# Kernel optimization log

Hardware: AMD Instinct MI355X
Metric: run time of the kernel (lower is better)

The kernel has to match this reference:

```python
import jax, jax.numpy as jnp
import numpy as np

B, T, D = 2, 2048, 1024
N, H = 16, 64  # num_heads, head_dim
LOG2E = 1.442695041
NEG_INF = -1.0e9


def setup_inputs() -> dict:
    key = jax.random.key(0)
    ks = jax.random.split(key, 6)
    return {
        "input_tensor": jax.random.normal(ks[0], (B, T, D), dtype=jnp.float32),
        "attention_mask": jax.random.randint(ks[1], (B, 1, T, T), 0, 2, dtype=jnp.int32),
        "wq": jax.random.normal(ks[2], (D, N, H), dtype=jnp.float32),
        "bq": jnp.zeros((N, H), dtype=jnp.float32),
        "wk": jax.random.normal(ks[3], (D, N, H), dtype=jnp.float32),
        "bk": jnp.zeros((N, H), dtype=jnp.float32),
        "wv": jax.random.normal(ks[4], (D, N, H), dtype=jnp.float32),
        "bv": jnp.zeros((N, H), dtype=jnp.float32),
        "wo": jax.random.normal(ks[5], (D, N, H), dtype=jnp.float32),
        "bo": jnp.zeros((D,), dtype=jnp.float32),
        "per_dim_scale": jnp.zeros((H,), dtype=jnp.float32),
    }


def reference(input_tensor, attention_mask, wq, bq, wk, bk, wv, bv, wo, bo, per_dim_scale):
    # QKV projections: [B,T,D] x [D,N,H] -> [B,T,N,H]
    q = jnp.einsum('btd,dnh->btnh', input_tensor, wq) + bq
    k = jnp.einsum('btd,dnh->btnh', input_tensor, wk) + bk
    v = jnp.einsum('btd,dnh->btnh', input_tensor, wv) + bv
    # per-dim query scaling: (log2(e)/sqrt(H)) * softplus(per_dim_scale)
    scale = (LOG2E / jnp.sqrt(jnp.asarray(H, q.dtype))) * jax.nn.softplus(per_dim_scale)
    q = q * scale
    # scores: [B,N,T,S]
    scores = jnp.einsum('btnh,bsnh->bnts', q, k)
    scores = jnp.where(attention_mask == 0, jnp.asarray(NEG_INF, scores.dtype), scores)
    weights = jax.nn.softmax(scores, axis=-1)
    # AV: [B,N,T,S] x [B,S,N,H] -> [B,T,N,H]
    attn_out = jnp.einsum('bnts,bsnh->btnh', weights, v)
    # output projection: [B,T,N,H] x [D,N,H] -> [B,T,D]
    return jnp.einsum('btnh,dnh->btd', attn_out, wo) + bo
```

## Files before the change

### kernel.cpp

```cpp
#include <hip/hip_runtime.h>
#include <math.h>

typedef __bf16 bf16;
typedef __attribute__((ext_vector_type(8))) __bf16 bf16x8;
typedef __attribute__((ext_vector_type(4))) __bf16 bf16x4;
typedef __attribute__((ext_vector_type(4))) float f32x4;

#define BB 2
#define TT 2048
#define DD 1024
#define NHD 16
#define HD 64
#define MM (BB*TT)
#define LOG2E_F 1.442695041f
#define NEGINF_F (-1.0e9f)

__device__ __forceinline__ void gld16(const bf16* g, bf16* l)
{
    __builtin_amdgcn_global_load_lds(
        (const __attribute__((address_space(1))) unsigned int*)g,
        (__attribute__((address_space(3))) unsigned int*)l, 16, 0, 0);
}

__global__ __launch_bounds__(256)
void prep_all(const float* __restrict__ X, const int* __restrict__ m,
              const float* __restrict__ wq, const float* __restrict__ wk,
              const float* __restrict__ wv, const float* __restrict__ wo,
              bf16* __restrict__ Xh, bf16* __restrict__ Xl,
              bf16* __restrict__ qkh, bf16* __restrict__ qkl,
              bf16* __restrict__ vh, bf16* __restrict__ ob,
              unsigned char* __restrict__ bits)
{
    __shared__ float tile[32][33];
    const int bid = blockIdx.x;
    const int t   = threadIdx.x;

    if (bid < 4096) {
        int i = bid * 256 + t;
        float4 v = ((const float4*)X)[i];
        float f[4] = {v.x, v.y, v.z, v.w};
        bf16x4 h, l;
        #pragma unroll
        for (int j = 0; j < 4; ++j) {
            bf16 hh = (bf16)f[j];
            h[j] = hh;
            l[j] = (bf16)(f[j] - (float)hh);
        }
        *(bf16x4*)(Xh + (size_t)i * 4) = h;
        *(bf16x4*)(Xl + (size_t)i * 4) = l;
        return;
    }
    if (bid < 8192) {
        const int idx = bid - 4096;
        const int z   = idx >> 10;
        const int bx  = (idx & 31) << 5;
        const int by  = ((idx >> 5) & 31) << 5;
        const int r   = t >> 3;
        const int c4  = (t & 7) << 2;
        if (z == 3) {
            float4 v = *(const float4*)(wo + (size_t)(by + r) * 1024 + bx + c4);
            bf16x4 o = { (bf16)v.x, (bf16)v.y, (bf16)v.z, (bf16)v.w };
            *(bf16x4*)(ob + (size_t)(by + r) * 1024 + bx + c4) = o;
            return;
        }
        const float* src = (z == 0) ? wq : ((z == 1) ? wk : wv);
        bf16* oh = (z == 0) ? qkh : ((z == 1) ? qkh + 1048576 : vh);
        bf16* ol = (z == 0) ? qkl : ((z == 1) ? qkl + 1048576 : nullptr);
        float4 v = *(const float4*)(src + (size_t)(by + r) * 1024 + bx + c4);
        tile[r][c4+0] = v.x; tile[r][c4+1] = v.y;
        tile[r][c4+2] = v.z; tile[r][c4+3] = v.w;
        __syncthreads();
        bf16x4 hv, lv;
        #pragma unroll
        for (int j = 0; j < 4; ++j) {
            float f = tile[c4 + j][r];
            bf16 h = (bf16)f;
            hv[j] = h;
            lv[j] = (bf16)(f - (float)h);
        }
        *(bf16x4*)(oh + (size_t)(bx + r) * 1024 + by + c4) = hv;
        if (ol)
            *(bf16x4*)(ol + (size_t)(bx + r) * 1024 + by + c4) = lv;
        return;
    }
    {
        int i = (bid - 8192) * 256 + t;
        const int4* mp = (const int4*)m + (size_t)i * 2;
        int4 a  = mp[0];
        int4 b4 = mp[1];
        unsigned v = (a.x  != 0)       | ((a.y  != 0) << 1)
                   | ((a.z  != 0) << 2) | ((a.w  != 0) << 3)
                   | ((b4.x != 0) << 4) | ((b4.y != 0) << 5)
                   | ((b4.z != 0) << 6) | ((b4.w != 0) << 7);
        bits[i] = (unsigned char)v;
    }
}

__global__ __launch_bounds__(256)
void gemm_proj(const bf16* __restrict__ Xh, const bf16* __restrict__ Xl,
               const bf16* __restrict__ Wh, const bf16* __restrict__ Wl,
               const bf16* __restrict__ Wvh,
               const float* __restrict__ bq, const float* __restrict__ bk,
               const float* __restrict__ bv, const float* __restrict__ pds,
               bf16* __restrict__ oQh, bf16* __restrict__ oQl,
               bf16* __restrict__ oKh, bf16* __restrict__ oKl,
               bf16* __restrict__ oVt)
{
    __shared__ bf16 S[4][128 * 32];

    const int bid  = blockIdx.x;
    const int t    = threadIdx.x;
    const int lane = t & 63;
    const int w    = t >> 6;
    const int quad = lane >> 4, l15 = lane & 15;
    const int wm   = (w >> 1) << 6;
    const int wn   = (w & 1)  << 6;

    const int jr0 = ((w * 2 + 0) << 4) + (lane >> 2);
    const int jr1 = ((w * 2 + 1) << 4) + (lane >> 2);
    const int kch = (lane & 3) << 3;
    const int off0 = (w * 2 + 0) * 512;
    const int off1 = (w * 2 + 1) * 512;

    if (bid < 512) {
        const int m0 = (bid >> 4) << 7;
        const int n0 = (bid & 15) << 7;
        bf16* Ah = S[0]; bf16* Al = S[1]; bf16* Bh = S[2]; bf16* Bl = S[3];

        const bf16* pAh0 = Xh + (size_t)(m0 + jr0) * DD + kch;
        const bf16* pAh1 = Xh + (size_t)(m0 + jr1) * DD + kch;
        const bf16* pAl0 = Xl + (size_t)(m0 + jr0) * DD + kch;
        const bf16* pAl1 = Xl + (size_t)(m0 + jr1) * DD + kch;
        const bf16* pBh0 = Wh + (size_t)(n0 + jr0) * DD + kch;
        const bf16* pBh1 = Wh + (size_t)(n0 + jr1) * DD + kch;
        const bf16* pBl0 = Wl + (size_t)(n0 + jr0) * DD + kch;
        const bf16* pBl1 = Wl + (size_t)(n0 + jr1) * DD + kch;

        f32x4 acc[4][4] = {};

        for (int k0 = 0; k0 < DD; k0 += 32) {
            __syncthreads();
            gld16(pAh0 + k0, Ah + off0);  gld16(pAh1 + k0, Ah + off1);
            gld16(pAl0 + k0, Al + off0);  gld16(pAl1 + k0, Al + off1);
            gld16(pBh0 + k0, Bh + off0);  gld16(pBh1 + k0, Bh + off1);
            gld16(pBl0 + k0, Bl + off0);  gld16(pBl1 + k0, Bl + off1);
            __syncthreads();

            bf16x8 ah[4], bh[4];
            #pragma unroll
            for (int mt = 0; mt < 4; ++mt)
                ah[mt] = *(const bf16x8*)(Ah + (wm + (mt << 4) + l15) * 32 + (quad << 3));
            #pragma unroll
            for (int nt = 0; nt < 4; ++nt)
                bh[nt] = *(const bf16x8*)(Bh + (wn + (nt << 4) + l15) * 32 + (quad << 3));
            #pragma unroll
            for (int mt = 0; mt < 4; ++mt)
                #pragma unroll
                for (int nt = 0; nt < 4; ++nt)
                    acc[mt][nt] = __builtin_amdgcn_mfma_f32_16x16x32_bf16(
                        ah[mt], bh[nt], acc[mt][nt], 0, 0, 0);

            bf16x8 bl[4];
            #pragma unroll
            for (int nt = 0; nt < 4; ++nt)
                bl[nt] = *(const bf16x8*)(Bl + (wn + (nt << 4) + l15) * 32 + (quad << 3));
            #pragma unroll
            for (int mt = 0; mt < 4; ++mt)
                #pragma unroll
                for (int nt = 0; nt < 4; ++nt)
                    acc[mt][nt] = __builtin_amdgcn_mfma_f32_16x16x32_bf16(
                        ah[mt], bl[nt], acc[mt][nt], 0, 0, 0);

            bf16x8 al[4];
            #pragma unroll
            for (int mt = 0; mt < 4; ++mt)
                al[mt] = *(const bf16x8*)(Al + (wm + (mt << 4) + l15) * 32 + (quad << 3));
            #pragma unroll
            for (int mt = 0; mt < 4; ++mt)
                #pragma unroll
                for (int nt = 0; nt < 4; ++nt)
                    acc[mt][nt] = __builtin_amdgcn_mfma_f32_16x16x32_bf16(
                        al[mt], bh[nt], acc[mt][nt], 0, 0, 0);
        }

        #pragma unroll
        for (int nt = 0; nt < 4; ++nt) {
            const int col = n0 + wn + (nt << 4) + l15;
            const int isQ = (col < 1024);
            const int nh  = col & 1023;
            const int n   = nh >> 6, h = nh & 63;
            const float bcol = isQ ? bq[nh] : bk[nh];
            float s = 1.f;
            if (isQ) {
                float x  = pds[h];
                float sp = fmaxf(x, 0.f) + log1pf(expf(-fabsf(x)));
                s = (LOG2E_F * LOG2E_F / 8.0f) * sp;
            }
            bf16* dH = isQ ? oQh : oKh;
            bf16* dL = isQ ? oQl : oKl;
            #pragma unroll
            for (int mt = 0; mt < 4; ++mt) {
                #pragma unroll
                for (int reg = 0; reg < 4; ++reg) {
                    const int row = m0 + wm + (mt << 4) + (quad << 2) + reg;
                    const int bi  = row >> 11;
                    const int tt  = row & (TT - 1);
                    float val = (acc[mt][nt][reg] + bcol) * s;
                    const size_t idx = (((size_t)bi * NHD + n) * TT + tt) * HD + h;
                    bf16 hi = (bf16)val;
                    dH[idx] = hi;
                    dL[idx] = (bf16)(val - (float)hi);
                }
            }
        }
    } else {
        const int idx = bid - 512;
        const int m0  = (idx >> 5) << 7;
        const int n0  = (idx & 31) << 7;
        bf16* As = S[0]; bf16* Bs = S[2];

        const bf16* Ap0 = Wvh + (size_t)(m0 + jr0) * DD + kch;
        const bf16* Ap1 = Wvh + (size_t)(m0 + jr1) * DD + kch;
        const bf16* Bp0 = Xh  + (size_t)(n0 + jr0) * DD + kch;
        const bf16* Bp1 = Xh  + (size_t)(n0 + jr1) * DD + kch;

        f32x4 acc[4][4] = {};

        for (int k0 = 0; k0 < DD; k0 += 32) {
            __syncthreads();
            gld16(Ap0 + k0, As + off0);
            gld16(Ap1 + k0, As + off1);
            gld16(Bp0 + k0, Bs + off0);
            gld16(Bp1 + k0, Bs + off1);
            __syncthreads();
            bf16x8 af[4], bfm[4];
            #pragma unroll
            for (int mt = 0; mt < 4; ++mt)
                af[mt] = *(const bf16x8*)(As + (wm + (mt << 4) + l15) * 32 + (quad << 3));
            #pragma unroll
            for (int nt = 0; nt < 4; ++nt)
                bfm[nt] = *(const bf16x8*)(Bs + (wn + (nt << 4) + l15) * 32 + (quad << 3));
            #pragma unroll
            for (int mt = 0; mt < 4; ++mt)
                #pragma unroll
                for (int nt = 0; nt < 4; ++nt)
                    acc[mt][nt] = __builtin_amdgcn_mfma_f32_16x16x32_bf16(
                        af[mt], bfm[nt], acc[mt][nt], 0, 0, 0);
        }

        #pragma unroll
        for (int nt = 0; nt < 4; ++nt) {
            const int col = n0 + wn + (nt << 4) + l15;
            const int bi  = col >> 11;
            const int tt  = col & (TT - 1);
            #pragma unroll
            for (int mt = 0; mt < 4; ++mt) {
                #pragma unroll
                for (int reg = 0; reg < 4; ++reg) {
                    const int row = m0 + wm + (mt << 4) + (quad << 2) + reg;
                    float val = acc[mt][nt][reg] + bv[row];
                    oVt[((size_t)bi * 1024 + row) * TT + tt] = (bf16)val;
                }
            }
        }
    }
}

__global__ __launch_bounds__(256)
void gemm_out(const bf16* __restrict__ A, const bf16* __restrict__ Bt,
              const float* __restrict__ bias, float* __restrict__ oF)
{
    __shared__ bf16 As[128 * 32];
    __shared__ bf16 Bs[64 * 32];

    const int t    = threadIdx.x;
    const int lane = t & 63;
    const int w    = t >> 6;
    const int quad = lane >> 4, l15 = lane & 15;
    const int m0   = blockIdx.y << 7;
    const int n0   = blockIdx.x << 6;
    const int wm   = (w >> 1) << 6;
    const int wn   = (w & 1)  << 5;

    const int jr0 = ((w * 2 + 0) << 4) + (lane >> 2);
    const int jr1 = ((w * 2 + 1) << 4) + (lane >> 2);
    const int jrB = (w << 4) + (lane >> 2);
    const int kch = (lane & 3) << 3;

    bf16* lA0 = As + (w * 2 + 0) * 512;
    bf16* lA1 = As + (w * 2 + 1) * 512;
    bf16* lB  = Bs + w * 512;

    const bf16* Ap0 = A  + (size_t)(m0 + jr0) * DD + kch;
    const bf16* Ap1 = A  + (size_t)(m0 + jr1) * DD + kch;
    const bf16* Bp  = Bt + (size_t)(n0 + jrB) * DD + kch;

    f32x4 acc[4][2] = {};

    for (int k0 = 0; k0 < DD; k0 += 32) {
        __syncthreads();
        gld16(Ap0 + k0, lA0);
        gld16(Ap1 + k0, lA1);
        gld16(Bp + k0, lB);
        __syncthreads();
        bf16x8 af[4], bfm[2];
        #pragma unroll
        for (int mt = 0; mt < 4; ++mt)
            af[mt] = *(const bf16x8*)(As + (wm + (mt << 4) + l15) * 32 + (quad << 3));
        #pragma unroll
        for (int nt = 0; nt < 2; ++nt)
            bfm[nt] = *(const bf16x8*)(Bs + (wn + (nt << 4) + l15) * 32 + (quad << 3));
        #pragma unroll
        for (int mt = 0; mt < 4; ++mt)
            #pragma unroll
            for (int nt = 0; nt < 2; ++nt)
                acc[mt][nt] = __builtin_amdgcn_mfma_f32_16x16x32_bf16(
                    af[mt], bfm[nt], acc[mt][nt], 0, 0, 0);
    }

    #pragma unroll
    for (int nt = 0; nt < 2; ++nt) {
        const int col = n0 + wn + (nt << 4) + l15;
        const float bcol = bias[col];
        #pragma unroll
        for (int mt = 0; mt < 4; ++mt) {
            #pragma unroll
            for (int reg = 0; reg < 4; ++reg) {
                const int row = m0 + wm + (mt << 4) + (quad << 2) + reg;
                oF[(size_t)row * DD + col] = acc[mt][nt][reg] + bcol;
            }
        }
    }
}

__global__ __launch_bounds__(512)
void attn_mfma(const bf16* __restrict__ Qh, const bf16* __restrict__ Ql,
               const bf16* __restrict__ Kh, const bf16* __restrict__ Kl,
               const bf16* __restrict__ Vt,
               const unsigned long long* __restrict__ mb64,
               bf16* __restrict__ AO)
{
    __shared__ bf16 Ksh[64][72];
    __shared__ bf16 Ksl[64][72];
    __shared__ bf16 Vts[64][72];
    __shared__ bf16 Ps[8][16][72];
    __shared__ unsigned long long msk64[128];

    const int t    = threadIdx.x;
    const int lane = t & 63;
    const int w    = t >> 6;
    const int quad = lane >> 4, l15 = lane & 15;
    const int bn   = blockIdx.y;
    const int b    = bn >> 4, n = bn & 15;
    const int q0   = blockIdx.x << 7;

    const bf16* Qbh = Qh + (size_t)bn * TT * HD;
    const bf16* Qbl = Ql + (size_t)bn * TT * HD;
    const bf16* Kbh = Kh + (size_t)bn * TT * HD;
    const bf16* Kbl = Kl + (size_t)bn * TT * HD;
    const bf16* Vtb = Vt + (size_t)bn * HD * TT;

    const int qrow = q0 + (w << 4) + l15;
    bf16x8 qfh[2], qfl[2];
    qfh[0] = *(const bf16x8*)(Qbh + (size_t)qrow * HD + (quad << 3));
    qfh[1] = *(const bf16x8*)(Qbh + (size_t)qrow * HD + 32 + (quad << 3));
    qfl[0] = *(const bf16x8*)(Qbl + (size_t)qrow * HD + (quad << 3));
    qfl[1] = *(const bf16x8*)(Qbl + (size_t)qrow * HD + 32 + (quad << 3));

    f32x4 O[4];
    #pragma unroll
    for (int i = 0; i < 4; ++i) O[i] = (f32x4){0.f,0.f,0.f,0.f};
    float m_i = -INFINITY;
    float l_i = 0.f;

    const int rS = t >> 3;
    const int cS = (((t & 7) ^ (rS & 7)) << 3);

    for (int kb = 0; kb < TT; kb += 64) {
        bf16x8 khv = *(const bf16x8*)(Kbh + (size_t)(kb + rS) * HD + cS);
        bf16x8 klv = *(const bf16x8*)(Kbl + (size_t)(kb + rS) * HD + cS);
        bf16x8 vv  = *(const bf16x8*)(Vtb + (size_t)rS * TT + kb + cS);
        unsigned long long mw = 0;
        if (t < 128)
            mw = mb64[((size_t)b * TT + q0 + t) * (TT / 64) + (kb >> 6)];

        __syncthreads();
        *(bf16x8*)&Ksh[rS][cS] = khv;
        *(bf16x8*)&Ksl[rS][cS] = klv;
        *(bf16x8*)&Vts[rS][cS] = vv;
        if (t < 128) msk64[t] = mw;
        __syncthreads();

        f32x4 s_acc[4];
        #pragma unroll
        for (int i = 0; i < 4; ++i) s_acc[i] = (f32x4){0.f,0.f,0.f,0.f};
        #pragma unroll
        for (int k2 = 0; k2 < 2; ++k2) {
            #pragma unroll
            for (int nt = 0; nt < 4; ++nt) {
                bf16x8 bkh = *(const bf16x8*)&Ksh[(nt << 4) + l15][(k2 << 5) + (quad << 3)];
                bf16x8 bkl = *(const bf16x8*)&Ksl[(nt << 4) + l15][(k2 << 5) + (quad << 3)];
                s_acc[nt] = __builtin_amdgcn_mfma_f32_16x16x32_bf16(bkh, qfh[k2], s_acc[nt], 0, 0, 0);
                s_acc[nt] = __builtin_amdgcn_mfma_f32_16x16x32_bf16(bkl, qfh[k2], s_acc[nt], 0, 0, 0);
                s_acc[nt] = __builtin_amdgcn_mfma_f32_16x16x32_bf16(bkh, qfl[k2], s_acc[nt], 0, 0, 0);
            }
        }

        const unsigned long long word = msk64[(w << 4) + l15];
        const unsigned w0 = (unsigned)word;
        const unsigned w1 = (unsigned)(word >> 32);
        float sv[16];
        #pragma unroll
        for (int nt = 0; nt < 4; ++nt) {
            const unsigned wrd = (nt & 2) ? w1 : w0;
            #pragma unroll
            for (int reg = 0; reg < 4; ++reg) {
                const int bit = ((nt & 1) << 4) + (quad << 2) + reg;
                sv[nt * 4 + reg] = ((wrd >> bit) & 1u) ? s_acc[nt][reg] : NEGINF_F;
            }
        }
        float mx = sv[0];
        #pragma unroll
        for (int i = 1; i < 16; ++i) mx = fmaxf(mx, sv[i]);
        mx = fmaxf(mx, __shfl_xor(mx, 16));
        mx = fmaxf(mx, __shfl_xor(mx, 32));
        const float mnew  = fmaxf(m_i, mx);
        const float alpha = exp2f(m_i - mnew);
        float p[16], sum = 0.f;
        #pragma unroll
        for (int i = 0; i < 16; ++i) { p[i] = exp2f(sv[i] - mnew); sum += p[i]; }
        sum += __shfl_xor(sum, 16);
        sum += __shfl_xor(sum, 32);
        l_i = l_i * alpha + sum;
        m_i = mnew;
        #pragma unroll
        for (int nt = 0; nt < 4; ++nt) {
            O[nt][0] *= alpha; O[nt][1] *= alpha;
            O[nt][2] *= alpha; O[nt][3] *= alpha;
            bf16x4 pv = { (bf16)p[nt * 4 + 0], (bf16)p[nt * 4 + 1],
                          (bf16)p[nt * 4 + 2], (bf16)p[nt * 4 + 3] };
            *(bf16x4*)&Ps[w][l15][(nt << 4) + (quad << 2)] = pv;
        }

        #pragma unroll
        for (int s2 = 0; s2 < 2; ++s2) {
            bf16x8 ap = *(const bf16x8*)&Ps[w][l15][(s2 << 5) + (quad << 3)];
            #pragma unroll
            for (int nt = 0; nt < 4; ++nt) {
                bf16x8 bv = *(const bf16x8*)&Vts[(nt << 4) + l15][(s2 << 5) + (quad << 3)];
                O[nt] = __builtin_amdgcn_mfma_f32_16x16x32_bf16(bv, ap, O[nt], 0, 0, 0);
            }
        }
    }

    {
        const float inv = 1.0f / l_i;
        const size_t base = ((size_t)b * TT + qrow) * (NHD * HD) + (size_t)n * HD;
        #pragma unroll
        for (int nt = 0; nt < 4; ++nt) {
            bf16x4 o = { (bf16)(O[nt][0] * inv), (bf16)(O[nt][1] * inv),
                         (bf16)(O[nt][2] * inv), (bf16)(O[nt][3] * inv) };
            *(bf16x4*)(AO + base + (nt << 4) + (quad << 2)) = o;
        }
    }
}

extern "C" void kernel_launch(void* const* d_in, const int* in_sizes, int n_in,
                              void* d_out, int out_size, void* d_ws, size_t ws_size,
                              hipStream_t stream)
{
    const float* X   = (const float*)d_in[0];
    const int*   msk = (const int*)d_in[1];
    const float* wq  = (const float*)d_in[2];
    const float* bq  = (const float*)d_in[3];
    const float* wk  = (const float*)d_in[4];
    const float* bk  = (const float*)d_in[5];
    const float* wv  = (const float*)d_in[6];
    const float* bv  = (const float*)d_in[7];
    const float* wo  = (const float*)d_in[8];
    const float* bo  = (const float*)d_in[9];
    const float* pds = (const float*)d_in[10];
    float* out = (float*)d_out;

    bf16* ws   = (bf16*)d_ws;
    bf16* Xh   = ws;
    bf16* Xl   = ws + 4194304;
    bf16* WQKh = ws + 8388608;
    bf16* WQKl = ws + 10485760;
    bf16* Wvh  = ws + 12582912;
    bf16* Wob  = ws + 13631488;
    bf16* Qhb  = ws + 14680064;
    bf16* Qlb  = ws + 18874368;
    bf16* Khb  = ws + 23068672;
    bf16* Klb  = ws + 27262976;
    unsigned char* mbits = (unsigned char*)(ws + 31457280);
    bf16* Vtb  = ws + 32505856;
    bf16* AOb  = Xh;

    dim3 blk(256);

    prep_all<<<12288, blk, 0, stream>>>(X, msk, wq, wk, wv, wo,
                                        Xh, Xl, WQKh, WQKl, Wvh, Wob, mbits);

    gemm_proj<<<768, blk, 0, stream>>>(
        Xh, Xl, WQKh, WQKl, Wvh, bq, bk, bv, pds,
        Qhb, Qlb, Khb, Klb, Vtb);

    dim3 ga(TT / 128, BB * NHD);
    attn_mfma<<<ga, dim3(512), 0, stream>>>(
        Qhb, Qlb, Khb, Klb, Vtb, (const unsigned long long*)mbits, AOb);

    gemm_out<<<dim3(16, 32), blk, 0, stream>>>(AOb, Wob, bo, out);
}
```

Measured before the change: 308.9 us.

## Swizzle attention LDS tiles, lazily rescale softmax, raise MFMA wave priority

The padded LDS tiles are replaced with unpadded 64-wide tiles that use an XOR swizzle on both stores and MFMA operand reads, to avoid bank conflicts while using less shared memory. Online-softmax rescaling is skipped when the block max exceeds the running max by no more than 8 in log2 units, so the O and l rescale runs less often. The max and sum reductions become tree-shaped, and s_setprio raises wave priority around the MFMA sections. The lazy rescale allows unnormalised exponentials up to 2^8, which reduces bf16 precision headroom in P.

```diff
diff --git a/kernel.cpp b/kernel.cpp
--- a/kernel.cpp
+++ b/kernel.cpp
@@ -340,10 +340,10 @@
                const unsigned long long* __restrict__ mb64,
                bf16* __restrict__ AO)
 {
-    __shared__ bf16 Ksh[64][72];
-    __shared__ bf16 Ksl[64][72];
-    __shared__ bf16 Vts[64][72];
-    __shared__ bf16 Ps[8][16][72];
+    __shared__ bf16 Ksh[64][64];
+    __shared__ bf16 Ksl[64][64];
+    __shared__ bf16 Vts[64][64];
+    __shared__ bf16 Ps[8][16][64];
     __shared__ unsigned long long msk64[128];
 
     const int t    = threadIdx.x;
@@ -374,37 +374,41 @@
     float l_i = 0.f;
 
     const int rS = t >> 3;
-    const int cS = (((t & 7) ^ (rS & 7)) << 3);
+    const int cG = (t & 7) << 3;
+    const int cL = (((t & 7) ^ (rS & 7)) << 3);
+    const int sw8 = (l15 & 7) << 3;
 
     for (int kb = 0; kb < TT; kb += 64) {
-        bf16x8 khv = *(const bf16x8*)(Kbh + (size_t)(kb + rS) * HD + cS);
-        bf16x8 klv = *(const bf16x8*)(Kbl + (size_t)(kb + rS) * HD + cS);
-        bf16x8 vv  = *(const bf16x8*)(Vtb + (size_t)rS * TT + kb + cS);
+        bf16x8 khv = *(const bf16x8*)(Kbh + (size_t)(kb + rS) * HD + cG);
+        bf16x8 klv = *(const bf16x8*)(Kbl + (size_t)(kb + rS) * HD + cG);
+        bf16x8 vv  = *(const bf16x8*)(Vtb + (size_t)rS * TT + kb + cG);
         unsigned long long mw = 0;
         if (t < 128)
             mw = mb64[((size_t)b * TT + q0 + t) * (TT / 64) + (kb >> 6)];
 
         __syncthreads();
-        *(bf16x8*)&Ksh[rS][cS] = khv;
-        *(bf16x8*)&Ksl[rS][cS] = klv;
-        *(bf16x8*)&Vts[rS][cS] = vv;
+        *(bf16x8*)&Ksh[rS][cL] = khv;
+        *(bf16x8*)&Ksl[rS][cL] = klv;
+        *(bf16x8*)&Vts[rS][cL] = vv;
         if (t < 128) msk64[t] = mw;
         __syncthreads();
 
         f32x4 s_acc[4];
         #pragma unroll
         for (int i = 0; i < 4; ++i) s_acc[i] = (f32x4){0.f,0.f,0.f,0.f};
+        __builtin_amdgcn_s_setprio(1);
         #pragma unroll
         for (int k2 = 0; k2 < 2; ++k2) {
             #pragma unroll
             for (int nt = 0; nt < 4; ++nt) {
-                bf16x8 bkh = *(const bf16x8*)&Ksh[(nt << 4) + l15][(k2 << 5) + (quad << 3)];
-                bf16x8 bkl = *(const bf16x8*)&Ksl[(nt << 4) + l15][(k2 << 5) + (quad << 3)];
+                bf16x8 bkh = *(const bf16x8*)&Ksh[(nt << 4) + l15][((k2 << 5) + (quad << 3)) ^ sw8];
+                bf16x8 bkl = *(const bf16x8*)&Ksl[(nt << 4) + l15][((k2 << 5) + (quad << 3)) ^ sw8];
                 s_acc[nt] = __builtin_amdgcn_mfma_f32_16x16x32_bf16(bkh, qfh[k2], s_acc[nt], 0, 0, 0);
                 s_acc[nt] = __builtin_amdgcn_mfma_f32_16x16x32_bf16(bkl, qfh[k2], s_acc[nt], 0, 0, 0);
                 s_acc[nt] = __builtin_amdgcn_mfma_f32_16x16x32_bf16(bkh, qfl[k2], s_acc[nt], 0, 0, 0);
             }
         }
+        __builtin_amdgcn_s_setprio(0);
 
         const unsigned long long word = msk64[(w << 4) + l15];
         const unsigned w0 = (unsigned)word;
@@ -419,38 +423,58 @@
                 sv[nt * 4 + reg] = ((wrd >> bit) & 1u) ? s_acc[nt][reg] : NEGINF_F;
             }
         }
-        float mx = sv[0];
-        #pragma unroll
-        for (int i = 1; i < 16; ++i) mx = fmaxf(mx, sv[i]);
+        float a0 = fmaxf(sv[0], sv[1]),  a1 = fmaxf(sv[2], sv[3]);
+        float a2 = fmaxf(sv[4], sv[5]),  a3 = fmaxf(sv[6], sv[7]);
+        float a4 = fmaxf(sv[8], sv[9]),  a5 = fmaxf(sv[10], sv[11]);
+        float a6 = fmaxf(sv[12], sv[13]), a7 = fmaxf(sv[14], sv[15]);
+        float b0 = fmaxf(a0, a1), b1 = fmaxf(a2, a3);
+        float b2 = fmaxf(a4, a5), b3 = fmaxf(a6, a7);
+        float mx = fmaxf(fmaxf(b0, b1), fmaxf(b2, b3));
         mx = fmaxf(mx, __shfl_xor(mx, 16));
         mx = fmaxf(mx, __shfl_xor(mx, 32));
-        const float mnew  = fmaxf(m_i, mx);
-        const float alpha = exp2f(m_i - mnew);
-        float p[16], sum = 0.f;
-        #pragma unroll
-        for (int i = 0; i < 16; ++i) { p[i] = exp2f(sv[i] - mnew); sum += p[i]; }
+
+        if (!__all(mx <= m_i + 8.0f)) {
+            const float mnew  = fmaxf(m_i, mx);
+            const float alpha = exp2f(m_i - mnew);
+            l_i *= alpha;
+            #pragma unroll
+            for (int nt = 0; nt < 4; ++nt) {
+                O[nt][0] *= alpha; O[nt][1] *= alpha;
+                O[nt][2] *= alpha; O[nt][3] *= alpha;
+            }
+            m_i = mnew;
+        }
+
+        float p[16];
+        #pragma unroll
+        for (int i = 0; i < 16; ++i) p[i] = exp2f(sv[i] - m_i);
+        float s0 = (p[0] + p[1]) + (p[2] + p[3]);
+        float s1 = (p[4] + p[5]) + (p[6] + p[7]);
+        float s2 = (p[8] + p[9]) + (p[10] + p[11]);
+        float s3 = (p[12] + p[13]) + (p[14] + p[15]);
+        float sum = (s0 + s1) + (s2 + s3);
         sum += __shfl_xor(sum, 16);
         sum += __shfl_xor(sum, 32);
-        l_i = l_i * alpha + sum;
-        m_i = mnew;
+        l_i += sum;
+
         #pragma unroll
         for (int nt = 0; nt < 4; ++nt) {
-            O[nt][0] *= alpha; O[nt][1] *= alpha;
-            O[nt][2] *= alpha; O[nt][3] *= alpha;
             bf16x4 pv = { (bf16)p[nt * 4 + 0], (bf16)p[nt * 4 + 1],
                           (bf16)p[nt * 4 + 2], (bf16)p[nt * 4 + 3] };
-            *(bf16x4*)&Ps[w][l15][(nt << 4) + (quad << 2)] = pv;
-        }
-
-        #pragma unroll
-        for (int s2 = 0; s2 < 2; ++s2) {
-            bf16x8 ap = *(const bf16x8*)&Ps[w][l15][(s2 << 5) + (quad << 3)];
+            *(bf16x4*)&Ps[w][l15][((nt << 4) + (quad << 2)) ^ sw8] = pv;
+        }
+
+        __builtin_amdgcn_s_setprio(1);
+        #pragma unroll
+        for (int s2i = 0; s2i < 2; ++s2i) {
+            bf16x8 ap = *(const bf16x8*)&Ps[w][l15][((s2i << 5) + (quad << 3)) ^ sw8];
             #pragma unroll
             for (int nt = 0; nt < 4; ++nt) {
-                bf16x8 bv = *(const bf16x8*)&Vts[(nt << 4) + l15][(s2 << 5) + (quad << 3)];
+                bf16x8 bv = *(const bf16x8*)&Vts[(nt << 4) + l15][((s2i << 5) + (quad << 3)) ^ sw8];
                 O[nt] = __builtin_amdgcn_mfma_f32_16x16x32_bf16(bv, ap, O[nt], 0, 0, 0);
             }
         }
+        __builtin_amdgcn_s_setprio(0);
     }
 
     {
```

Measured after the change: 312.9 us. About the same (+1.3%).
